# Kernel tuning notes

Measured on AMD Instinct MI355X. Metric: run time of the kernel, lower is better.

Reference implementation:

```python
import jax, jax.numpy as jnp
import numpy as np

N = 10000      # nodes
DIN = 1024     # input feature dim
H = 256        # hidden dim
NC = 3         # classes
EDGE_P = 0.002 # ~avg degree 20


def _lin(key, fin, fout):
    s = 1.0 / np.sqrt(fin)
    kw, kb = jax.random.split(key)
    W = jax.random.uniform(kw, (fin, fout), jnp.float32, -s, s)
    b = jax.random.uniform(kb, (fout,), jnp.float32, -s, s)
    return W, b


def setup_inputs() -> dict:
    key = jax.random.key(0)
    ks = jax.random.split(key, 10)
    features = jax.random.normal(ks[0], (N, DIN), jnp.float32)
    # sparse weighted adjacency with zero diagonal (dense storage, as the module expects)
    mask = jax.random.uniform(ks[1], (N, N)) < EDGE_P
    wts = jax.random.uniform(ks[2], (N, N), jnp.float32)
    adj = jnp.where(mask, wts, 0.0) * (1.0 - jnp.eye(N, dtype=jnp.float32))
    W0, b0 = _lin(ks[3], DIN, H)
    W1, b1 = _lin(ks[4], H, H)
    W2, b2 = _lin(ks[5], H, H)
    C1w, c1b = _lin(ks[6], 2 * H, H)
    C2w, c2b = _lin(ks[7], H, H // 2)
    C3w, c3b = _lin(ks[8], H // 2, NC)
    return {"features": features, "adj": adj,
            "W0": W0, "b0": b0, "W1": W1, "b1": b1, "W2": W2, "b2": b2,
            "C1w": C1w, "c1b": c1b, "C2w": C2w, "c2b": c2b, "C3w": C3w, "c3b": c3b}


def _gcn_norm(adj):
    # PyG GCNConv: add self-loops (weight 1), symmetric deg^{-1/2} normalization.
    A = adj + jnp.eye(adj.shape[0], dtype=adj.dtype)
    deg = A.sum(axis=1)
    dinv = jnp.where(deg > 0, jax.lax.rsqrt(deg), 0.0)
    return dinv[:, None] * A * dinv[None, :]


def reference(features, adj, W0, b0, W1, b1, W2, b2, C1w, c1b, C2w, c2b, C3w, c3b):
    An = _gcn_norm(adj)                       # [N, N] normalized adjacency
    x = features
    for W, b in ((W0, b0), (W1, b1), (W2, b2)):
        x = jax.nn.relu(An @ (x @ W) + b)     # linear -> aggregate -> bias -> relu
        # dropout is identity in eval mode
    g = jnp.concatenate([x.max(axis=0), x.mean(axis=0)])  # [2H]
    h = jax.nn.relu(g @ C1w + c1b)
    h = jax.nn.relu(h @ C2w + c2b)
    return h @ C3w + c3b                      # [NC] logits
```

## Files before the change

kernel.cpp:

```cpp
#include <hip/hip_runtime.h>
#include <hip/hip_bf16.h>

#define NN 10000
#define FDIN 1024
#define HH 256
#define CAP 64
#define MPAD 10112
#define WT_BLOCKS 1536
#define FCONV_BLOCKS 5000

typedef unsigned short u16;
typedef unsigned int u32;
typedef __attribute__((ext_vector_type(8))) short short8;
typedef __attribute__((ext_vector_type(4))) float f32x4;

__device__ __forceinline__ float ld_in(const void* p, size_t i, int bf) {
    if (bf) {
        unsigned short u = ((const unsigned short*)p)[i];
        return __uint_as_float(((unsigned int)u) << 16);
    }
    return ((const float*)p)[i];
}

__device__ __forceinline__ u16 bf16bits(float x) {
    __hip_bfloat16 h = __float2bfloat16(x);
    return *(u16*)&h;
}

__device__ __forceinline__ float bf16val(u16 u) {
    return __uint_as_float(((unsigned int)u) << 16);
}

__device__ __forceinline__ int local_flag(const void* feat, int tid, int* cnts) {
    u16 u = ((const u16*)feat)[2 * tid];
    int e = (u >> 7) & 0xFF;
    bool pred = (e >= 100 && e <= 137);
    unsigned long long b = __ballot(pred);
    if ((tid & 63) == 0) cnts[tid >> 6] = __popcll(b);
    __syncthreads();
    return (cnts[0] + cnts[1] + cnts[2] + cnts[3]) >= 128;
}

__global__ __launch_bounds__(256) void k_scanconv(const void* __restrict__ feat,
                                                  const void* __restrict__ adj,
                                                  const void* __restrict__ W0,
                                                  const void* __restrict__ W1,
                                                  const void* __restrict__ W2,
                                                  int* __restrict__ flag,
                                                  int* __restrict__ ellc,
                                                  float* __restrict__ ellv,
                                                  int* __restrict__ cnt,
                                                  float* __restrict__ dinv,
                                                  u16* __restrict__ featb,
                                                  u16* __restrict__ w0t,
                                                  u16* __restrict__ w1t,
                                                  u16* __restrict__ w2t) {
    __shared__ int cnts[4];
    __shared__ int s_cnt;
    __shared__ float s_sum;
    int tid = threadIdx.x;
    int bid = blockIdx.x;
    if (tid == 0) { s_cnt = 0; s_sum = 0.f; }
    int f = local_flag(feat, tid, cnts);
    if (bid == 0 && tid == 0) *flag = f;

    if (bid < NN) {
        int i = bid;
        float lsum = 0.f;
        if (f) {
            const uint4* p = (const uint4*)((const u16*)adj + (size_t)i * NN);
            for (int t = tid; t < NN / 8; t += 256) {
                uint4 q = p[t];
                if ((q.x | q.y | q.z | q.w) == 0u) continue;
                unsigned int w_[4] = {q.x, q.y, q.z, q.w};
                #pragma unroll
                for (int w = 0; w < 4; ++w) {
                    #pragma unroll
                    for (int hh = 0; hh < 2; ++hh) {
                        unsigned short u = (unsigned short)(w_[w] >> (16 * hh));
                        if (u) {
                            float v = bf16val(u);
                            lsum += v;
                            int slot = atomicAdd(&s_cnt, 1);
                            if (slot < CAP) {
                                ellc[(size_t)i * CAP + slot] = t * 8 + w * 2 + hh;
                                ellv[(size_t)i * CAP + slot] = v;
                            }
                        }
                    }
                }
            }
        } else {
            const uint4* p = (const uint4*)((const float*)adj + (size_t)i * NN);
            for (int t = tid; t < NN / 4; t += 256) {
                uint4 qi = p[t];
                if ((qi.x | qi.y | qi.z | qi.w) == 0u) continue;
                unsigned int w_[4] = {qi.x, qi.y, qi.z, qi.w};
                #pragma unroll
                for (int w = 0; w < 4; ++w) {
                    float v = __uint_as_float(w_[w]);
                    if (v != 0.f) {
                        lsum += v;
                        int slot = atomicAdd(&s_cnt, 1);
                        if (slot < CAP) {
                            ellc[(size_t)i * CAP + slot] = t * 4 + w;
                            ellv[(size_t)i * CAP + slot] = v;
                        }
                    }
                }
            }
        }
        for (int off = 32; off > 0; off >>= 1) lsum += __shfl_down(lsum, off, 64);
        if ((tid & 63) == 0) atomicAdd(&s_sum, lsum);
        __syncthreads();
        if (tid == 0) {
            float deg = s_sum + 1.0f;
            dinv[i] = rsqrtf(deg);
            cnt[i] = s_cnt < CAP ? s_cnt : CAP;
        }
        return;
    }
    if (bid < NN + WT_BLOCKS) {
        int idx = (bid - NN) * 256 + tid;
        const void* W; u16* Wt; int K;
        if (idx < FDIN * HH)                { W = W0; Wt = w0t; K = FDIN; }
        else if (idx < FDIN * HH + HH * HH) { W = W1; Wt = w1t; K = HH; idx -= FDIN * HH; }
        else                                { W = W2; Wt = w2t; K = HH; idx -= FDIN * HH + HH * HH; }
        int k = idx >> 8, n = idx & 255;
        Wt[(size_t)n * K + k] = bf16bits(ld_in(W, (size_t)idx, f));
        return;
    }
    if (f) return;
    int idx = (bid - NN - WT_BLOCKS) * 256 + tid;
    int row = idx >> 7;
    int c0 = (idx & 127) * 8;
    const float* fp = (const float*)feat + (size_t)row * FDIN + c0;
    float4 v0 = *(const float4*)fp;
    float4 v1 = *(const float4*)(fp + 4);
    float vv[8] = {v0.x, v0.y, v0.z, v0.w, v1.x, v1.y, v1.z, v1.w};
    u16 outv[8];
    #pragma unroll
    for (int e = 0; e < 8; ++e) outv[e] = bf16bits(vv[e]);
    *(uint4*)(featb + (size_t)row * FDIN + c0) = *(const uint4*)outv;
}


__device__ __forceinline__ void g_load(const u16* A, const u16* Bt, int K, int m0, int n0,
                                       int tid, int k0, uint4* sa, uint4* sb) {
    #pragma unroll
    for (int q = 0; q < 2; ++q) {
        int c = q * 256 + tid, row = c >> 3, b = (c & 7) << 4;
        uint4 v = {0u, 0u, 0u, 0u};
        if (m0 + row < NN)
            v = *(const uint4*)((const unsigned char*)(A + (size_t)(m0 + row) * K + k0) + b);
        sa[q] = v;
    }
    #pragma unroll
    for (int q = 0; q < 4; ++q) {
        int c = q * 256 + tid, n = c >> 3, b = (c & 7) << 4;
        sb[q] = *(const uint4*)((const unsigned char*)(Bt + (size_t)(n0 + n) * K + k0) + b);
    }
}

__device__ __forceinline__ void lds_store(unsigned char* Asb, unsigned char* Bsb, int tid,
                                          const uint4* sa, const uint4* sb) {
    #pragma unroll
    for (int q = 0; q < 2; ++q) {
        int c = q * 256 + tid, row = c >> 3, b = (c & 7) << 4;
        *(uint4*)(Asb + row * 128 + (b ^ ((row & 7) << 4))) = sa[q];
    }
    #pragma unroll
    for (int q = 0; q < 4; ++q) {
        int c = q * 256 + tid, n = c >> 3, b = (c & 7) << 4;
        *(uint4*)(Bsb + n * 128 + (b ^ ((n & 7) << 4))) = sb[q];
    }
}

__device__ __forceinline__ void compute64(const unsigned char* Asb, const unsigned char* Bsb,
                                          int l, int wm, int wn, f32x4 acc[2][4]) {
    #pragma unroll
    for (int kk = 0; kk < 2; ++kk) {
        int kb = kk * 64 + ((l >> 4) << 4);
        short8 av[2], bv[4];
        #pragma unroll
        for (int i = 0; i < 2; ++i) {
            int row = wm * 32 + i * 16 + (l & 15);
            av[i] = *(const short8*)(Asb + row * 128 + (kb ^ ((row & 7) << 4)));
        }
        #pragma unroll
        for (int j = 0; j < 4; ++j) {
            int n = wn * 64 + j * 16 + (l & 15);
            bv[j] = *(const short8*)(Bsb + n * 128 + (kb ^ ((n & 7) << 4)));
        }
        #pragma unroll
        for (int i = 0; i < 2; ++i)
            #pragma unroll
            for (int j = 0; j < 4; ++j)
                acc[i][j] = __builtin_amdgcn_mfma_f32_16x16x32_bf16(av[i], bv[j], acc[i][j], 0, 0, 0);
    }
}

__global__ __launch_bounds__(256) void k_mfma(const u16* __restrict__ A1,
                                              const u16* __restrict__ A2,
                                              const u16* __restrict__ Bt,
                                              const int* __restrict__ flag,
                                              u16* __restrict__ Y, int K) {
    __shared__ uint4 As4[512];
    __shared__ uint4 Bs4[1024];
    unsigned char* Asb = (unsigned char*)As4;
    unsigned char* Bsb = (unsigned char*)Bs4;
    const u16* A = (*flag) ? A1 : A2;
    const int tid = threadIdx.x;
    const int l = tid & 63;
    const int wid = tid >> 6;
    const int wm = wid >> 1, wn = wid & 1;
    const int m0 = blockIdx.y * 64;
    const int n0 = blockIdx.x * 128;

    f32x4 acc[2][4] = {};
    uint4 sa[2], sb[4], ta[2], tb[4];
    g_load(A, Bt, K, m0, n0, tid, 0, sa, sb);
    const int nt = K >> 6;
    for (int t = 0; t < nt; t += 2) {
        __syncthreads();
        lds_store(Asb, Bsb, tid, sa, sb);
        __syncthreads();
        g_load(A, Bt, K, m0, n0, tid, (t + 1) << 6, ta, tb);
        compute64(Asb, Bsb, l, wm, wn, acc);
        __syncthreads();
        lds_store(Asb, Bsb, tid, ta, tb);
        __syncthreads();
        if (t + 2 < nt) g_load(A, Bt, K, m0, n0, tid, (t + 2) << 6, sa, sb);
        compute64(Asb, Bsb, l, wm, wn, acc);
    }
    #pragma unroll
    for (int i = 0; i < 2; ++i) {
        int r0 = m0 + wm * 32 + i * 16 + ((l >> 4) << 2);
        #pragma unroll
        for (int j = 0; j < 4; ++j) {
            int col = n0 + wn * 64 + j * 16 + (l & 15);
            #pragma unroll
            for (int r = 0; r < 4; ++r)
                Y[(size_t)(r0 + r) * HH + col] = bf16bits(acc[i][j][r]);
        }
    }
}

__global__ __launch_bounds__(128) void k_agg(const u32* __restrict__ y,
                                             const int* __restrict__ ellc,
                                             const float* __restrict__ ellv,
                                             const int* __restrict__ cnt,
                                             const float* __restrict__ dinv,
                                             const void* __restrict__ bias,
                                             const int* __restrict__ flag,
                                             u32* __restrict__ xout) {
    int i = blockIdx.x, j = threadIdx.x;
    int f = *flag;
    float di = dinv[i];
    u32 w = y[(size_t)i * 128 + j];
    float a0 = di * bf16val((u16)(w & 0xffff));
    float a1 = di * bf16val((u16)(w >> 16));
    int c_ = cnt[i];
    for (int e = 0; e < c_; ++e) {
        int c = ellc[(size_t)i * CAP + e];
        float s = ellv[(size_t)i * CAP + e] * dinv[c];
        u32 v = y[(size_t)c * 128 + j];
        a0 = fmaf(s, bf16val((u16)(v & 0xffff)), a0);
        a1 = fmaf(s, bf16val((u16)(v >> 16)), a1);
    }
    float v0 = fmaf(di, a0, ld_in(bias, (size_t)(2 * j), f));
    float v1 = fmaf(di, a1, ld_in(bias, (size_t)(2 * j + 1), f));
    v0 = v0 > 0.f ? v0 : 0.f;
    v1 = v1 > 0.f ? v1 : 0.f;
    xout[(size_t)i * 128 + j] = (u32)bf16bits(v0) | ((u32)bf16bits(v1) << 16);
}

__global__ __launch_bounds__(256) void k_pool(const u16* __restrict__ x,
                                              float* __restrict__ pmax,
                                              float* __restrict__ psum) {
    int j = threadIdx.x, b = blockIdx.x;
    int r0 = b * 250;
    float m = 0.f, s = 0.f;
    for (int r = r0; r < r0 + 250; ++r) {
        float v = bf16val(x[(size_t)r * HH + j]);
        m = fmaxf(m, v);
        s += v;
    }
    pmax[b * HH + j] = m;
    psum[b * HH + j] = s;
}

__global__ __launch_bounds__(256) void k_head(const float* __restrict__ pmax,
                                              const float* __restrict__ psum,
                                              const void* C1w, const void* c1b,
                                              const void* C2w, const void* c2b,
                                              const void* C3w, const void* c3b,
                                              const int* __restrict__ flag,
                                              void* __restrict__ out) {
    __shared__ float gs[2 * HH], h1[HH], h2[HH / 2];
    int j = threadIdx.x;
    int f = *flag;
    float m = 0.f, s = 0.f;
    #pragma unroll 4
    for (int b = 0; b < 40; ++b) {
        m = fmaxf(m, pmax[b * HH + j]);
        s += psum[b * HH + j];
    }
    gs[j] = m;
    gs[HH + j] = s * (1.0f / (float)NN);
    __syncthreads();
    float a = 0.f;
    for (int k = 0; k < 2 * HH; ++k) a = fmaf(gs[k], ld_in(C1w, (size_t)k * HH + j, f), a);
    a += ld_in(c1b, j, f);
    h1[j] = a > 0.f ? a : 0.f;
    __syncthreads();
    if (j < HH / 2) {
        float b2_ = 0.f;
        for (int k = 0; k < HH; ++k) b2_ = fmaf(h1[k], ld_in(C2w, (size_t)k * (HH / 2) + j, f), b2_);
        b2_ += ld_in(c2b, j, f);
        h2[j] = b2_ > 0.f ? b2_ : 0.f;
    }
    __syncthreads();
    if (j < 3) {
        float o = 0.f;
        for (int k = 0; k < HH / 2; ++k) o = fmaf(h2[k], ld_in(C3w, (size_t)k * 3 + j, f), o);
        o += ld_in(c3b, j, f);
        if (f) ((__hip_bfloat16*)out)[j] = __float2bfloat16(o);
        else   ((float*)out)[j] = o;
    }
}

extern "C" void kernel_launch(void* const* d_in, const int* in_sizes, int n_in,
                              void* d_out, int out_size, void* d_ws, size_t ws_size,
                              hipStream_t stream) {
    const void* feat = d_in[0];
    const void* adj  = d_in[1];
    const void* W0 = d_in[2];  const void* b0 = d_in[3];
    const void* W1 = d_in[4];  const void* b1 = d_in[5];
    const void* W2 = d_in[6];  const void* b2 = d_in[7];
    const void* C1w = d_in[8]; const void* c1b = d_in[9];
    const void* C2w = d_in[10]; const void* c2b = d_in[11];
    const void* C3w = d_in[12]; const void* c3b = d_in[13];

    char* ws = (char*)d_ws;
    size_t o = 0;
    auto take = [&](size_t bytes) -> void* {
        void* p = ws + o;
        o += (bytes + 255) & ~(size_t)255;
        return p;
    };
    int*   flag  = (int*)take(4);
    float* dinv  = (float*)take((size_t)NN * 4);
    int*   cnt   = (int*)take((size_t)NN * 4);
    int*   ellc  = (int*)take((size_t)NN * CAP * 4);
    float* ellv  = (float*)take((size_t)NN * CAP * 4);
    u16*   featb = (u16*)take((size_t)NN * FDIN * 2);
    u16*   w0t   = (u16*)take((size_t)HH * FDIN * 2);
    u16*   w1t   = (u16*)take((size_t)HH * HH * 2);
    u16*   w2t   = (u16*)take((size_t)HH * HH * 2);
    u16*   xbuf  = (u16*)take((size_t)MPAD * HH * 2);
    u16*   ybuf  = (u16*)take((size_t)MPAD * HH * 2);
    float* pmax  = (float*)take((size_t)40 * HH * 4);
    float* psum  = (float*)take((size_t)40 * HH * 4);

    k_scanconv<<<NN + WT_BLOCKS + FCONV_BLOCKS, 256, 0, stream>>>(
        feat, adj, W0, W1, W2, flag, ellc, ellv, cnt, dinv, featb, w0t, w1t, w2t);

    dim3 gg(2, MPAD / 64);
    k_mfma<<<gg, 256, 0, stream>>>((const u16*)feat, featb, w0t, flag, ybuf, FDIN);
    k_agg<<<NN, 128, 0, stream>>>((const u32*)ybuf, ellc, ellv, cnt, dinv, b0, flag, (u32*)xbuf);
    k_mfma<<<gg, 256, 0, stream>>>(xbuf, xbuf, w1t, flag, ybuf, HH);
    k_agg<<<NN, 128, 0, stream>>>((const u32*)ybuf, ellc, ellv, cnt, dinv, b1, flag, (u32*)xbuf);
    k_mfma<<<gg, 256, 0, stream>>>(xbuf, xbuf, w2t, flag, ybuf, HH);
    k_agg<<<NN, 128, 0, stream>>>((const u32*)ybuf, ellc, ellv, cnt, dinv, b2, flag, (u32*)xbuf);

    k_pool<<<40, 256, 0, stream>>>(xbuf, pmax, psum);
    k_head<<<1, 256, 0, stream>>>(pmax, psum, C1w, c1b, C2w, c2b, C3w, c3b, flag, d_out);
}
```

Baseline: 385.8 us.

## Fuse fp32-to-bf16 feature conversion into first GEMM and co-schedule with adjacency scan

Drops the separate pass that converts the feature matrix to bf16 and wrote it to a workspace buffer. The first GEMM now loads fp32 features and converts them on the fly. That GEMM runs as the first blocks of one kernel alongside the adjacency-scan blocks, so the two stages overlap. Weight transposition moves into its own small kernel that runs first. This saves a full write and re-read of the bf16 feature matrix, at the cost of wider fp32 loads inside the GEMM inner loop and a mixed-role kernel.

New measurement: 410.7 us. 1.06x slower.

```diff
diff --git a/kernel.cpp b/kernel.cpp
--- a/kernel.cpp
+++ b/kernel.cpp
@@ -7,7 +7,7 @@
 #define CAP 64
 #define MPAD 10112
 #define WT_BLOCKS 1536
-#define FCONV_BLOCKS 5000
+#define G1_BLOCKS 316
 
 typedef unsigned short u16;
 typedef unsigned int u32;
@@ -41,20 +41,138 @@
     return (cnts[0] + cnts[1] + cnts[2] + cnts[3]) >= 128;
 }
 
-__global__ __launch_bounds__(256) void k_scanconv(const void* __restrict__ feat,
-                                                  const void* __restrict__ adj,
-                                                  const void* __restrict__ W0,
-                                                  const void* __restrict__ W1,
-                                                  const void* __restrict__ W2,
-                                                  int* __restrict__ flag,
-                                                  int* __restrict__ ellc,
-                                                  float* __restrict__ ellv,
-                                                  int* __restrict__ cnt,
-                                                  float* __restrict__ dinv,
-                                                  u16* __restrict__ featb,
-                                                  u16* __restrict__ w0t,
-                                                  u16* __restrict__ w1t,
-                                                  u16* __restrict__ w2t) {
+__global__ __launch_bounds__(256) void k_wt(const void* __restrict__ feat,
+                                            const void* __restrict__ W0,
+                                            const void* __restrict__ W1,
+                                            const void* __restrict__ W2,
+                                            int* __restrict__ flag,
+                                            u16* __restrict__ w0t,
+                                            u16* __restrict__ w1t,
+                                            u16* __restrict__ w2t) {
+    __shared__ int cnts[4];
+    int tid = threadIdx.x;
+    int f = local_flag(feat, tid, cnts);
+    if (blockIdx.x == 0 && tid == 0) *flag = f;
+    int idx = blockIdx.x * 256 + tid;
+    const void* W; u16* Wt; int K;
+    if (idx < FDIN * HH)                { W = W0; Wt = w0t; K = FDIN; }
+    else if (idx < FDIN * HH + HH * HH) { W = W1; Wt = w1t; K = HH; idx -= FDIN * HH; }
+    else                                { W = W2; Wt = w2t; K = HH; idx -= FDIN * HH + HH * HH; }
+    int k = idx >> 8, n = idx & 255;
+    Wt[(size_t)n * K + k] = bf16bits(ld_in(W, (size_t)idx, f));
+}
+
+
+__device__ __forceinline__ void lds_store(unsigned char* Asb, unsigned char* Bsb, int tid,
+                                          const uint4* sa, const uint4* sb) {
+    #pragma unroll
+    for (int q = 0; q < 2; ++q) {
+        int c = q * 256 + tid, row = c >> 3, b = (c & 7) << 4;
+        *(uint4*)(Asb + row * 128 + (b ^ ((row & 7) << 4))) = sa[q];
+    }
+    #pragma unroll
+    for (int q = 0; q < 4; ++q) {
+        int c = q * 256 + tid, n = c >> 3, b = (c & 7) << 4;
+        *(uint4*)(Bsb + n * 128 + (b ^ ((n & 7) << 4))) = sb[q];
+    }
+}
+
+__device__ __forceinline__ void compute64(const unsigned char* Asb, const unsigned char* Bsb,
+                                          int l, int wm, int wn, f32x4 acc[2][4]) {
+    #pragma unroll
+    for (int kk = 0; kk < 2; ++kk) {
+        int kb = kk * 64 + ((l >> 4) << 4);
+        short8 av[2], bv[4];
+        #pragma unroll
+        for (int i = 0; i < 2; ++i) {
+            int row = wm * 32 + i * 16 + (l & 15);
+            av[i] = *(const short8*)(Asb + row * 128 + (kb ^ ((row & 7) << 4)));
+        }
+        #pragma unroll
+        for (int j = 0; j < 4; ++j) {
+            int n = wn * 64 + j * 16 + (l & 15);
+            bv[j] = *(const short8*)(Bsb + n * 128 + (kb ^ ((n & 7) << 4)));
+        }
+        #pragma unroll
+        for (int i = 0; i < 2; ++i)
+            #pragma unroll
+            for (int j = 0; j < 4; ++j)
+                acc[i][j] = __builtin_amdgcn_mfma_f32_16x16x32_bf16(av[i], bv[j], acc[i][j], 0, 0, 0);
+    }
+}
+
+__device__ __forceinline__ uint4 load_a(const void* A, int f, size_t row, int K, int e0) {
+    if (f) return *(const uint4*)((const u16*)A + row * K + e0);
+    const float* fp = (const float*)A + row * K + e0;
+    float4 v0 = *(const float4*)fp, v1 = *(const float4*)(fp + 4);
+    float4 v2 = *(const float4*)(fp + 8), v3 = *(const float4*)(fp + 12);
+    float vv[16] = {v0.x, v0.y, v0.z, v0.w, v1.x, v1.y, v1.z, v1.w,
+                    v2.x, v2.y, v2.z, v2.w, v3.x, v3.y, v3.z, v3.w};
+    u16 o[16];
+    #pragma unroll
+    for (int e = 0; e < 16; ++e) o[e] = bf16bits(vv[e]);
+    return *(const uint4*)o;
+}
+
+__device__ __forceinline__ void gemm_body(const void* A, int f, const u16* Bt,
+                                          u16* Y, int K, int m0, int n0, int tid,
+                                          unsigned char* Asb, unsigned char* Bsb) {
+    const int l = tid & 63;
+    const int wid = tid >> 6;
+    const int wm = wid >> 1, wn = wid & 1;
+    f32x4 acc[2][4] = {};
+    uint4 sa[2], sb[4], ta[2], tb[4];
+    auto g_load = [&](int k0, uint4* xa, uint4* xb) {
+        #pragma unroll
+        for (int q = 0; q < 2; ++q) {
+            int c = q * 256 + tid, row = c >> 3, e0 = (c & 7) << 3;
+            uint4 v = {0u, 0u, 0u, 0u};
+            if (m0 + row < NN) v = load_a(A, f, (size_t)(m0 + row), K, k0 + e0);
+            xa[q] = v;
+        }
+        #pragma unroll
+        for (int q = 0; q < 4; ++q) {
+            int c = q * 256 + tid, n = c >> 3, b = (c & 7) << 4;
+            xb[q] = *(const uint4*)((const unsigned char*)(Bt + (size_t)(n0 + n) * K + k0) + b);
+        }
+    };
+    g_load(0, sa, sb);
+    const int nt = K >> 6;
+    for (int t = 0; t < nt; t += 2) {
+        __syncthreads();
+        lds_store(Asb, Bsb, tid, sa, sb);
+        __syncthreads();
+        g_load((t + 1) << 6, ta, tb);
+        compute64(Asb, Bsb, l, wm, wn, acc);
+        __syncthreads();
+        lds_store(Asb, Bsb, tid, ta, tb);
+        __syncthreads();
+        if (t + 2 < nt) g_load((t + 2) << 6, sa, sb);
+        compute64(Asb, Bsb, l, wm, wn, acc);
+    }
+    #pragma unroll
+    for (int i = 0; i < 2; ++i) {
+        int r0 = m0 + wm * 32 + i * 16 + ((l >> 4) << 2);
+        #pragma unroll
+        for (int j = 0; j < 4; ++j) {
+            int col = n0 + wn * 64 + j * 16 + (l & 15);
+            #pragma unroll
+            for (int r = 0; r < 4; ++r)
+                Y[(size_t)(r0 + r) * HH + col] = bf16bits(acc[i][j][r]);
+        }
+    }
+}
+
+__global__ __launch_bounds__(256) void k_front(const void* __restrict__ feat,
+                                               const void* __restrict__ adj,
+                                               const u16* __restrict__ w0t,
+                                               u16* __restrict__ ybuf,
+                                               int* __restrict__ ellc,
+                                               float* __restrict__ ellv,
+                                               int* __restrict__ cnt,
+                                               float* __restrict__ dinv) {
+    __shared__ uint4 As4[512];
+    __shared__ uint4 Bs4[1024];
     __shared__ int cnts[4];
     __shared__ int s_cnt;
     __shared__ float s_sum;
@@ -62,188 +180,79 @@
     int bid = blockIdx.x;
     if (tid == 0) { s_cnt = 0; s_sum = 0.f; }
     int f = local_flag(feat, tid, cnts);
-    if (bid == 0 && tid == 0) *flag = f;
-
-    if (bid < NN) {
-        int i = bid;
-        float lsum = 0.f;
-        if (f) {
-            const uint4* p = (const uint4*)((const u16*)adj + (size_t)i * NN);
-            for (int t = tid; t < NN / 8; t += 256) {
-                uint4 q = p[t];
-                if ((q.x | q.y | q.z | q.w) == 0u) continue;
-                unsigned int w_[4] = {q.x, q.y, q.z, q.w};
+
+    if (bid < G1_BLOCKS) {
+        int m0 = (bid >> 1) * 64;
+        int n0 = (bid & 1) * 128;
+        gemm_body(feat, f, w0t, ybuf, FDIN, m0, n0, tid,
+                  (unsigned char*)As4, (unsigned char*)Bs4);
+        return;
+    }
+    int i = bid - G1_BLOCKS;
+    float lsum = 0.f;
+    if (f) {
+        const uint4* p = (const uint4*)((const u16*)adj + (size_t)i * NN);
+        for (int t = tid; t < NN / 8; t += 256) {
+            uint4 q = p[t];
+            if ((q.x | q.y | q.z | q.w) == 0u) continue;
+            unsigned int w_[4] = {q.x, q.y, q.z, q.w};
+            #pragma unroll
+            for (int w = 0; w < 4; ++w) {
                 #pragma unroll
-                for (int w = 0; w < 4; ++w) {
-                    #pragma unroll
-                    for (int hh = 0; hh < 2; ++hh) {
-                        unsigned short u = (unsigned short)(w_[w] >> (16 * hh));
-                        if (u) {
-                            float v = bf16val(u);
-                            lsum += v;
-                            int slot = atomicAdd(&s_cnt, 1);
-                            if (slot < CAP) {
-                                ellc[(size_t)i * CAP + slot] = t * 8 + w * 2 + hh;
-                                ellv[(size_t)i * CAP + slot] = v;
-                            }
-                        }
-                    }
-                }
-            }
-        } else {
-            const uint4* p = (const uint4*)((const float*)adj + (size_t)i * NN);
-            for (int t = tid; t < NN / 4; t += 256) {
-                uint4 qi = p[t];
-                if ((qi.x | qi.y | qi.z | qi.w) == 0u) continue;
-                unsigned int w_[4] = {qi.x, qi.y, qi.z, qi.w};
-                #pragma unroll
-                for (int w = 0; w < 4; ++w) {
-                    float v = __uint_as_float(w_[w]);
-                    if (v != 0.f) {
+                for (int hh = 0; hh < 2; ++hh) {
+                    unsigned short u = (unsigned short)(w_[w] >> (16 * hh));
+                    if (u) {
+                        float v = bf16val(u);
                         lsum += v;
                         int slot = atomicAdd(&s_cnt, 1);
                         if (slot < CAP) {
-                            ellc[(size_t)i * CAP + slot] = t * 4 + w;
+                            ellc[(size_t)i * CAP + slot] = t * 8 + w * 2 + hh;
                             ellv[(size_t)i * CAP + slot] = v;
                         }
                     }
                 }
             }
         }
-        for (int off = 32; off > 0; off >>= 1) lsum += __shfl_down(lsum, off, 64);
-        if ((tid & 63) == 0) atomicAdd(&s_sum, lsum);
-        __syncthreads();
-        if (tid == 0) {
-            float deg = s_sum + 1.0f;
-            dinv[i] = rsqrtf(deg);
-            cnt[i] = s_cnt < CAP ? s_cnt : CAP;
-        }
-        return;
-    }
-    if (bid < NN + WT_BLOCKS) {
-        int idx = (bid - NN) * 256 + tid;
-        const void* W; u16* Wt; int K;
-        if (idx < FDIN * HH)                { W = W0; Wt = w0t; K = FDIN; }
-        else if (idx < FDIN * HH + HH * HH) { W = W1; Wt = w1t; K = HH; idx -= FDIN * HH; }
-        else                                { W = W2; Wt = w2t; K = HH; idx -= FDIN * HH + HH * HH; }
-        int k = idx >> 8, n = idx & 255;
-        Wt[(size_t)n * K + k] = bf16bits(ld_in(W, (size_t)idx, f));
-        return;
-    }
-    if (f) return;
-    int idx = (bid - NN - WT_BLOCKS) * 256 + tid;
-    int row = idx >> 7;
-    int c0 = (idx & 127) * 8;
-    const float* fp = (const float*)feat + (size_t)row * FDIN + c0;
-    float4 v0 = *(const float4*)fp;
-    float4 v1 = *(const float4*)(fp + 4);
-    float vv[8] = {v0.x, v0.y, v0.z, v0.w, v1.x, v1.y, v1.z, v1.w};
-    u16 outv[8];
-    #pragma unroll
-    for (int e = 0; e < 8; ++e) outv[e] = bf16bits(vv[e]);
-    *(uint4*)(featb + (size_t)row * FDIN + c0) = *(const uint4*)outv;
-}
-
-
-__device__ __forceinline__ void g_load(const u16* A, const u16* Bt, int K, int m0, int n0,
-                                       int tid, int k0, uint4* sa, uint4* sb) {
-    #pragma unroll
-    for (int q = 0; q < 2; ++q) {
-        int c = q * 256 + tid, row = c >> 3, b = (c & 7) << 4;
-        uint4 v = {0u, 0u, 0u, 0u};
-        if (m0 + row < NN)
-            v = *(const uint4*)((const unsigned char*)(A + (size_t)(m0 + row) * K + k0) + b);
-        sa[q] = v;
-    }
-    #pragma unroll
-    for (int q = 0; q < 4; ++q) {
-        int c = q * 256 + tid, n = c >> 3, b = (c & 7) << 4;
-        sb[q] = *(const uint4*)((const unsigned char*)(Bt + (size_t)(n0 + n) * K + k0) + b);
-    }
-}
-
-__device__ __forceinline__ void lds_store(unsigned char* Asb, unsigned char* Bsb, int tid,
-                                          const uint4* sa, const uint4* sb) {
-    #pragma unroll
-    for (int q = 0; q < 2; ++q) {
-        int c = q * 256 + tid, row = c >> 3, b = (c & 7) << 4;
-        *(uint4*)(Asb + row * 128 + (b ^ ((row & 7) << 4))) = sa[q];
-    }
-    #pragma unroll
-    for (int q = 0; q < 4; ++q) {
-        int c = q * 256 + tid, n = c >> 3, b = (c & 7) << 4;
-        *(uint4*)(Bsb + n * 128 + (b ^ ((n & 7) << 4))) = sb[q];
-    }
-}
-
-__device__ __forceinline__ void compute64(const unsigned char* Asb, const unsigned char* Bsb,
-                                          int l, int wm, int wn, f32x4 acc[2][4]) {
-    #pragma unroll
-    for (int kk = 0; kk < 2; ++kk) {
-        int kb = kk * 64 + ((l >> 4) << 4);
-        short8 av[2], bv[4];
-        #pragma unroll
-        for (int i = 0; i < 2; ++i) {
-            int row = wm * 32 + i * 16 + (l & 15);
-            av[i] = *(const short8*)(Asb + row * 128 + (kb ^ ((row & 7) << 4)));
-        }
-        #pragma unroll
-        for (int j = 0; j < 4; ++j) {
-            int n = wn * 64 + j * 16 + (l & 15);
-            bv[j] = *(const short8*)(Bsb + n * 128 + (kb ^ ((n & 7) << 4)));
-        }
-        #pragma unroll
-        for (int i = 0; i < 2; ++i)
+    } else {
+        const uint4* p = (const uint4*)((const float*)adj + (size_t)i * NN);
+        for (int t = tid; t < NN / 4; t += 256) {
+            uint4 qi = p[t];
+            if ((qi.x | qi.y | qi.z | qi.w) == 0u) continue;
+            unsigned int w_[4] = {qi.x, qi.y, qi.z, qi.w};
             #pragma unroll
-            for (int j = 0; j < 4; ++j)
-                acc[i][j] = __builtin_amdgcn_mfma_f32_16x16x32_bf16(av[i], bv[j], acc[i][j], 0, 0, 0);
-    }
-}
-
-__global__ __launch_bounds__(256) void k_mfma(const u16* __restrict__ A1,
-                                              const u16* __restrict__ A2,
+            for (int w = 0; w < 4; ++w) {
+                float v = __uint_as_float(w_[w]);
+                if (v != 0.f) {
+                    lsum += v;
+                    int slot = atomicAdd(&s_cnt, 1);
+                    if (slot < CAP) {
+                        ellc[(size_t)i * CAP + slot] = t * 4 + w;
+                        ellv[(size_t)i * CAP + slot] = v;
+                    }
+                }
+            }
+        }
+    }
+    for (int off = 32; off > 0; off >>= 1) lsum += __shfl_down(lsum, off, 64);
+    if ((tid & 63) == 0) atomicAdd(&s_sum, lsum);
+    __syncthreads();
+    if (tid == 0) {
+        float deg = s_sum + 1.0f;
+        dinv[i] = rsqrtf(deg);
+        cnt[i] = s_cnt < CAP ? s_cnt : CAP;
+    }
+}
+
+__global__ __launch_bounds__(256) void k_mfma(const u16* __restrict__ A,
                                               const u16* __restrict__ Bt,
-                                              const int* __restrict__ flag,
                                               u16* __restrict__ Y, int K) {
     __shared__ uint4 As4[512];
     __shared__ uint4 Bs4[1024];
-    unsigned char* Asb = (unsigned char*)As4;
-    unsigned char* Bsb = (unsigned char*)Bs4;
-    const u16* A = (*flag) ? A1 : A2;
-    const int tid = threadIdx.x;
-    const int l = tid & 63;
-    const int wid = tid >> 6;
-    const int wm = wid >> 1, wn = wid & 1;
-    const int m0 = blockIdx.y * 64;
-    const int n0 = blockIdx.x * 128;
-
-    f32x4 acc[2][4] = {};
-    uint4 sa[2], sb[4], ta[2], tb[4];
-    g_load(A, Bt, K, m0, n0, tid, 0, sa, sb);
-    const int nt = K >> 6;
-    for (int t = 0; t < nt; t += 2) {
-        __syncthreads();
-        lds_store(Asb, Bsb, tid, sa, sb);
-        __syncthreads();
-        g_load(A, Bt, K, m0, n0, tid, (t + 1) << 6, ta, tb);
-        compute64(Asb, Bsb, l, wm, wn, acc);
-        __syncthreads();
-        lds_store(Asb, Bsb, tid, ta, tb);
-        __syncthreads();
-        if (t + 2 < nt) g_load(A, Bt, K, m0, n0, tid, (t + 2) << 6, sa, sb);
-        compute64(Asb, Bsb, l, wm, wn, acc);
-    }
-    #pragma unroll
-    for (int i = 0; i < 2; ++i) {
-        int r0 = m0 + wm * 32 + i * 16 + ((l >> 4) << 2);
-        #pragma unroll
-        for (int j = 0; j < 4; ++j) {
-            int col = n0 + wn * 64 + j * 16 + (l & 15);
-            #pragma unroll
-            for (int r = 0; r < 4; ++r)
-                Y[(size_t)(r0 + r) * HH + col] = bf16bits(acc[i][j][r]);
-        }
-    }
+    int tid = threadIdx.x;
+    int m0 = blockIdx.y * 64;
+    int n0 = blockIdx.x * 128;
+    gemm_body(A, 1, Bt, Y, K, m0, n0, tid,
+              (unsigned char*)As4, (unsigned char*)Bs4);
 }
 
 __global__ __launch_bounds__(128) void k_agg(const u32* __restrict__ y,
@@ -354,7 +363,6 @@
     int*   cnt   = (int*)take((size_t)NN * 4);
     int*   ellc  = (int*)take((size_t)NN * CAP * 4);
     float* ellv  = (float*)take((size_t)NN * CAP * 4);
-    u16*   featb = (u16*)take((size_t)NN * FDIN * 2);
     u16*   w0t   = (u16*)take((size_t)HH * FDIN * 2);
     u16*   w1t   = (u16*)take((size_t)HH * HH * 2);
     u16*   w2t   = (u16*)take((size_t)HH * HH * 2);
@@ -363,15 +371,15 @@
     float* pmax  = (float*)take((size_t)40 * HH * 4);
     float* psum  = (float*)take((size_t)40 * HH * 4);
 
-    k_scanconv<<<NN + WT_BLOCKS + FCONV_BLOCKS, 256, 0, stream>>>(
-        feat, adj, W0, W1, W2, flag, ellc, ellv, cnt, dinv, featb, w0t, w1t, w2t);
+    k_wt<<<WT_BLOCKS, 256, 0, stream>>>(feat, W0, W1, W2, flag, w0t, w1t, w2t);
+    k_front<<<G1_BLOCKS + NN, 256, 0, stream>>>(feat, adj, w0t, ybuf,
+                                                ellc, ellv, cnt, dinv);
 
     dim3 gg(2, MPAD / 64);
-    k_mfma<<<gg, 256, 0, stream>>>((const u16*)feat, featb, w0t, flag, ybuf, FDIN);
     k_agg<<<NN, 128, 0, stream>>>((const u32*)ybuf, ellc, ellv, cnt, dinv, b0, flag, (u32*)xbuf);
-    k_mfma<<<gg, 256, 0, stream>>>(xbuf, xbuf, w1t, flag, ybuf, HH);
+    k_mfma<<<gg, 256, 0, stream>>>(xbuf, w1t, ybuf, HH);
     k_agg<<<NN, 128, 0, stream>>>((const u32*)ybuf, ellc, ellv, cnt, dinv, b1, flag, (u32*)xbuf);
-    k_mfma<<<gg, 256, 0, stream>>>(xbuf, xbuf, w2t, flag, ybuf, HH);
+    k_mfma<<<gg, 256, 0, stream>>>(xbuf, w2t, ybuf, HH);
     k_agg<<<NN, 128, 0, stream>>>((const u32*)ybuf, ellc, ellv, cnt, dinv, b2, flag, (u32*)xbuf);
 
     k_pool<<<40, 256, 0, stream>>>(xbuf, pmax, psum);
```

## Stage GEMM tiles straight into LDS with a double-buffered pipeline

Applied to the files above, without the earlier changes.

The MFMA GEMM now uses global_load_lds to copy A and B tiles directly from global memory into LDS. The XOR swizzle moves into the global source address. LDS is double-buffered, so the next tile's load is issued before computing on the current one, with one barrier per k-step instead of four barriers per two steps. This removes the register staging and the extra LDS store instructions. Out-of-range A rows are clamped to the last row rather than zero-filled, which relies on the padded output rows being ignored.

Measured after the change: 338.1 us (median of 2 runs). -12.4%, faster.

```diff
diff --git a/kernel.cpp b/kernel.cpp
--- a/kernel.cpp
+++ b/kernel.cpp
@@ -29,6 +29,11 @@
 
 __device__ __forceinline__ float bf16val(u16 u) {
     return __uint_as_float(((unsigned int)u) << 16);
+}
+
+__device__ __forceinline__ void gload16(const void* g, void* l) {
+    __builtin_amdgcn_global_load_lds((const __attribute__((address_space(1))) void*)g,
+                                     (__attribute__((address_space(3))) void*)l, 16, 0, 0);
 }
 
 __device__ __forceinline__ int local_flag(const void* feat, int tid, int* cnts) {
@@ -145,37 +150,6 @@
 }
 
 
-__device__ __forceinline__ void g_load(const u16* A, const u16* Bt, int K, int m0, int n0,
-                                       int tid, int k0, uint4* sa, uint4* sb) {
-    #pragma unroll
-    for (int q = 0; q < 2; ++q) {
-        int c = q * 256 + tid, row = c >> 3, b = (c & 7) << 4;
-        uint4 v = {0u, 0u, 0u, 0u};
-        if (m0 + row < NN)
-            v = *(const uint4*)((const unsigned char*)(A + (size_t)(m0 + row) * K + k0) + b);
-        sa[q] = v;
-    }
-    #pragma unroll
-    for (int q = 0; q < 4; ++q) {
-        int c = q * 256 + tid, n = c >> 3, b = (c & 7) << 4;
-        sb[q] = *(const uint4*)((const unsigned char*)(Bt + (size_t)(n0 + n) * K + k0) + b);
-    }
-}
-
-__device__ __forceinline__ void lds_store(unsigned char* Asb, unsigned char* Bsb, int tid,
-                                          const uint4* sa, const uint4* sb) {
-    #pragma unroll
-    for (int q = 0; q < 2; ++q) {
-        int c = q * 256 + tid, row = c >> 3, b = (c & 7) << 4;
-        *(uint4*)(Asb + row * 128 + (b ^ ((row & 7) << 4))) = sa[q];
-    }
-    #pragma unroll
-    for (int q = 0; q < 4; ++q) {
-        int c = q * 256 + tid, n = c >> 3, b = (c & 7) << 4;
-        *(uint4*)(Bsb + n * 128 + (b ^ ((n & 7) << 4))) = sb[q];
-    }
-}
-
 __device__ __forceinline__ void compute64(const unsigned char* Asb, const unsigned char* Bsb,
                                           int l, int wm, int wn, f32x4 acc[2][4]) {
     #pragma unroll
@@ -205,10 +179,9 @@
                                               const u16* __restrict__ Bt,
                                               const int* __restrict__ flag,
                                               u16* __restrict__ Y, int K) {
-    __shared__ uint4 As4[512];
-    __shared__ uint4 Bs4[1024];
-    unsigned char* Asb = (unsigned char*)As4;
-    unsigned char* Bsb = (unsigned char*)Bs4;
+    __shared__ uint4 lds4[3072];
+    unsigned char* Abase = (unsigned char*)lds4;
+    unsigned char* Bbase = Abase + 16384;
     const u16* A = (*flag) ? A1 : A2;
     const int tid = threadIdx.x;
     const int l = tid & 63;
@@ -216,22 +189,39 @@
     const int wm = wid >> 1, wn = wid & 1;
     const int m0 = blockIdx.y * 64;
     const int n0 = blockIdx.x * 128;
+    const int bofs = ((l & 7) ^ (l >> 3)) << 4;
+    const int rsub = l >> 3;
+    const size_t Kb = (size_t)K * 2;
 
     f32x4 acc[2][4] = {};
-    uint4 sa[2], sb[4], ta[2], tb[4];
-    g_load(A, Bt, K, m0, n0, tid, 0, sa, sb);
+    auto stage = [&](int k0, int buf) {
+        unsigned char* Ab = Abase + (buf << 13);
+        unsigned char* Bb = Bbase + (buf << 14);
+        int kB = k0 << 1;
+        #pragma unroll
+        for (int q = 0; q < 2; ++q) {
+            int i = wid + (q << 2);
+            int row = m0 + (i << 3) + rsub;
+            if (row > NN - 1) row = NN - 1;
+            gload16((const unsigned char*)A + (size_t)row * Kb + kB + bofs,
+                    Ab + (i << 10));
+        }
+        #pragma unroll
+        for (int q = 0; q < 4; ++q) {
+            int i = wid + (q << 2);
+            int n = n0 + (i << 3) + rsub;
+            gload16((const unsigned char*)Bt + (size_t)n * Kb + kB + bofs,
+                    Bb + (i << 10));
+        }
+    };
+
+    stage(0, 0);
     const int nt = K >> 6;
-    for (int t = 0; t < nt; t += 2) {
+    __syncthreads();
+    for (int t = 0; t < nt; ++t) {
+        if (t + 1 < nt) stage((t + 1) << 6, (t + 1) & 1);
+        compute64(Abase + ((t & 1) << 13), Bbase + ((t & 1) << 14), l, wm, wn, acc);
         __syncthreads();
-        lds_store(Asb, Bsb, tid, sa, sb);
-        __syncthreads();
-        g_load(A, Bt, K, m0, n0, tid, (t + 1) << 6, ta, tb);
-        compute64(Asb, Bsb, l, wm, wn, acc);
-        __syncthreads();
-        lds_store(Asb, Bsb, tid, ta, tb);
-        __syncthreads();
-        if (t + 2 < nt) g_load(A, Bt, K, m0, n0, tid, (t + 2) << 6, sa, sb);
-        compute64(Asb, Bsb, l, wm, wn, acc);
     }
     #pragma unroll
     for (int i = 0; i < 2; ++i) {
```
